# Performance work log

Hardware: AMD Instinct MI355X
Metric: run time of the kernel (lower is better)

The kernel has to match this reference:

```python
import jax, jax.numpy as jnp
import numpy as np

B, N, DIM = 4, 4096, 768
H = 12
DH = DIM // H          # 64
S = 16                 # num_segments
M = N // S             # 256 segment_len
SCALE = DH ** -0.5


def setup_inputs() -> dict:
    key = jax.random.key(0)
    ks = jax.random.split(key, 7)
    std = DIM ** -0.5
    return {
        "x": jax.random.normal(ks[0], (B, N, DIM), dtype=jnp.float32),
        "Wq": jax.random.normal(ks[1], (DIM, DIM), dtype=jnp.float32) * std,
        "Wkv": jax.random.normal(ks[2], (DIM, DIM), dtype=jnp.float32) * std,
        "Wo": jax.random.normal(ks[3], (DIM, DIM), dtype=jnp.float32) * std,
        "bo": jax.random.normal(ks[4], (DIM,), dtype=jnp.float32) * 0.02,
        "Wo0": jax.random.normal(ks[5], (DIM, DIM), dtype=jnp.float32) * std,
        "bo0": jax.random.normal(ks[6], (DIM,), dtype=jnp.float32) * 0.02,
    }


def _rotary_freqs(n, dh, dtype):
    # lucidrains RotaryEmbedding: inv_freq over even dims, emb = cat(freqs, freqs)
    inv_freq = 1.0 / (10000.0 ** (jnp.arange(0, dh, 2, dtype=jnp.float32) / dh))
    t = jnp.arange(n, dtype=jnp.float32)
    freqs = jnp.einsum("n,f->nf", t, inv_freq)           # (n, dh/2)
    return jnp.concatenate([freqs, freqs], axis=-1).astype(dtype)  # (n, dh)


def _rotate_half(t):
    # '... (j d) -> ... j d', j=2 ; (-x2, x1)
    x1, x2 = jnp.split(t, 2, axis=-1)
    return jnp.concatenate([-x2, x1], axis=-1)


def _apply_rotary(freqs, t):
    # freqs: (1, n, dh) broadcast over (bh, n, dh); rot_dim == dh here
    return t * jnp.cos(freqs) + _rotate_half(t) * jnp.sin(freqs)


def reference(x, Wq, Wkv, Wo, bo, Wo0, bo0):
    b, n, dim = x.shape
    q = x @ Wq            # (b, n, dim), bias-free
    kv = x @ Wkv          # shared K==V projection

    def to_heads(t):      # 'b n (h d) -> (b h) n d'
        return t.reshape(b, n, H, DH).transpose(0, 2, 1, 3).reshape(b * H, n, DH)

    q, kv = to_heads(q), to_heads(kv)

    freqs = _rotary_freqs(n, DH, x.dtype)[None, :, :]    # (1, n, dh)
    q = _apply_rotary(freqs, q)
    kv = _apply_rotary(freqs, kv)

    q = q * SCALE
    c = b * H
    qs = q.reshape(c, S, M, DH)
    kvs = kv.reshape(c, S, M, DH)

    # adjacent-segment KV windows: segment t attends to [t-1, t] for t>=1
    kvs_ccs = jnp.concatenate([kvs[:, :-1], kvs[:, 1:]], axis=2)  # (c, S-1, 2M, dh)
    qs_ccs = qs[:, 1:]                                            # (c, S-1, M, dh)

    lsim = jnp.einsum("csmd,csnd->csmn", qs_ccs, kvs_ccs)         # (c, S-1, M, 2M)
    attn1 = jax.nn.softmax(lsim, axis=-1)
    out1 = jnp.einsum("csmn,csnd->csmd", attn1, kvs_ccs)          # (c, S-1, M, dh)

    # global (self) attention within first segment
    q0, kv0 = qs[:, 0], kvs[:, 0]                                 # (c, M, dh)
    sim0 = jnp.einsum("cmd,cnd->cmn", q0, kv0)
    attn0 = jax.nn.softmax(sim0, axis=-1)
    out0 = jnp.einsum("cmn,cnd->cmd", attn0, kv0)                 # (c, M, dh)

    def merge_heads(t, nn):  # '(b h) nn d -> b nn (h d)'
        return t.reshape(b, H, nn, DH).transpose(0, 2, 1, 3).reshape(b, nn, H * DH)

    out_1 = merge_heads(out1.reshape(c, (S - 1) * M, DH), (S - 1) * M)
    out_0 = merge_heads(out0, M)

    out_1o = out_1 @ Wo + bo
    out_0o = out_0 @ Wo0 + bo0
    return jnp.concatenate([out_0o, out_1o], axis=1)              # (b, n, dim)
```

## Files before the change

### kernel.cpp

```cpp
#include <hip/hip_runtime.h>
#include <hip/hip_bf16.h>


typedef float f32x4 __attribute__((ext_vector_type(4)));
typedef short bf16x8 __attribute__((ext_vector_type(8)));

#define DEV static __device__ __forceinline__

DEV short f2bf(float f) {
  union { __hip_bfloat16 h; unsigned short u; } cv;
  cv.h = __float2bfloat16(f);
  return (short)cv.u;
}

DEV f32x4 fz4() { f32x4 z = {0.f, 0.f, 0.f, 0.f}; return z; }

DEV void gload16(const void* g, void* l) {
  __builtin_amdgcn_global_load_lds((const __attribute__((address_space(1))) void*)g,
                                   (__attribute__((address_space(3))) void*)l, 16, 0, 0);
}

__global__ void __launch_bounds__(256) k_rope(float2* __restrict__ csT) {
  int idx = blockIdx.x * 256 + threadIdx.x;
  int pos = idx >> 5, jm = idx & 31;
  float invf = exp2f(-(float)jm * (13.287712379549449f / 32.0f));
  float th = (float)pos * invf;
  csT[idx] = make_float2(cosf(th), sinf(th));
}

__global__ void __launch_bounds__(256) k_cvtx(const float* __restrict__ x,
                                              short* __restrict__ xb) {
  int i = (blockIdx.x * 256 + threadIdx.x) * 8;
  float4 a = *(const float4*)(x + i);
  float4 b = *(const float4*)(x + i + 4);
  bf16x8 v;
  v[0] = f2bf(a.x); v[1] = f2bf(a.y); v[2] = f2bf(a.z); v[3] = f2bf(a.w);
  v[4] = f2bf(b.x); v[5] = f2bf(b.y); v[6] = f2bf(b.z); v[7] = f2bf(b.w);
  *(bf16x8*)(xb + i) = v;
}

__global__ void __launch_bounds__(256) k_transw(const float* __restrict__ Wq,
                                                const float* __restrict__ Wkv,
                                                const float* __restrict__ Wo,
                                                const float* __restrict__ Wo0,
                                                short* __restrict__ WtQKV,
                                                short* __restrict__ WtO) {
  __shared__ float t[64][65];
  int z = blockIdx.z;
  const float* src = (z == 0) ? Wq : (z == 1) ? Wkv : (z == 2) ? Wo : Wo0;
  short* dst = (z < 2) ? (WtQKV + (size_t)z * (768 * 768))
                       : (WtO + (size_t)(z - 2) * (768 * 768));
  int k0 = blockIdx.x * 64, j0 = blockIdx.y * 64;
  int tc = threadIdx.x & 63, tr = threadIdx.x >> 6;
#pragma unroll
  for (int i = 0; i < 16; i++) {
    int r = i * 4 + tr;
    t[tc][r] = src[(size_t)(k0 + r) * 768 + j0 + tc];
  }
  __syncthreads();
#pragma unroll
  for (int i = 0; i < 16; i++) {
    int r = i * 4 + tr;
    dst[(size_t)(j0 + r) * 768 + k0 + tc] = f2bf(t[r][tc]);
  }
}

#define QSTAGE64(Abuf, Bbuf, Abase, Bbase, kt)                                 \
  {                                                                            \
    int cci = (((tid & 7) ^ ((tid >> 3) & 7)) << 4);                           \
    _Pragma("unroll") for (int i = 0; i < 4; i++) {                            \
      int rowi = i * 32 + (tid >> 3);                                          \
      gload16((Abase) + (size_t)(r0 + rowi) * 1536 + (kt) * 128 + cci,         \
              (char*)(Abuf) + i * 4096 + wid * 1024);                          \
      gload16((Bbase) + (size_t)(j0 + rowi) * 1536 + (kt) * 128 + cci,         \
              (char*)(Bbuf) + i * 4096 + wid * 1024);                          \
    }                                                                          \
  }

__global__ void __launch_bounds__(256, 2) k_gemm_qkv(
    const short* __restrict__ xb, const short* __restrict__ Wt,
    const float2* __restrict__ csT,
    short* __restrict__ Qb, short* __restrict__ KVb,
    short* __restrict__ KVtw) {
  __shared__ short Lsh[4][8192];
  int bid = blockIdx.x;
  int xcd = bid & 7, loc = bid >> 3;
  int r0 = (xcd * 16 + loc / 12) * 128;
  int cbk = loc % 12;
  bool isQ = cbk < 6;
  int cbl = isQ ? cbk : cbk - 6;
  const char* Ab = (const char*)xb;
  const char* Bb = (const char*)(Wt + (isQ ? (size_t)0 : (size_t)(768 * 768)));
  int j0 = cbl * 128;
  int tid = threadIdx.x, lane = tid & 63, wid = tid >> 6;
  int wr = wid >> 1, wc = wid & 1;
  int l15 = lane & 15, lg = lane >> 4;
  int swz = (l15 & 7) << 4;

  f32x4 acc[4][4];
#pragma unroll
  for (int i = 0; i < 4; i++)
#pragma unroll
    for (int j = 0; j < 4; j++) acc[i][j] = fz4();

  QSTAGE64(Lsh[0], Lsh[2], Ab, Bb, 0)
  for (int kt = 0; kt < 12; kt++) {
    int cb = kt & 1;
    __syncthreads();
    if (kt + 1 < 12) QSTAGE64(Lsh[cb ^ 1], Lsh[2 + (cb ^ 1)], Ab, Bb, kt + 1)
    const char* Ac = (const char*)Lsh[cb];
    const char* Bc = (const char*)Lsh[2 + cb];
#pragma unroll
    for (int kk = 0; kk < 2; kk++) {
      bf16x8 af[4], bfr[4];
#pragma unroll
      for (int mr = 0; mr < 4; mr++)
        af[mr] = *(const bf16x8*)(Ac + (wr * 64 + mr * 16 + l15) * 128 +
                                  ((kk * 64 + lg * 16) ^ swz));
#pragma unroll
      for (int nc = 0; nc < 4; nc++)
        bfr[nc] = *(const bf16x8*)(Bc + (wc * 64 + nc * 16 + l15) * 128 +
                                   ((kk * 64 + lg * 16) ^ swz));
#pragma unroll
      for (int mr = 0; mr < 4; mr++)
#pragma unroll
        for (int nc = 0; nc < 4; nc++)
          acc[mr][nc] = __builtin_amdgcn_mfma_f32_16x16x32_bf16(af[mr], bfr[nc], acc[mr][nc], 0, 0, 0);
    }
  }

  int h = 2 * cbl + wc;
  short* Ob = isQ ? Qb : KVb;
  float scl = isQ ? 0.18033688011112042f : 1.0f;
  short ovv[4][4][4];
#pragma unroll
  for (int mr = 0; mr < 4; mr++) {
#pragma unroll
    for (int rg = 0; rg < 4; rg++) {
      int r = r0 + wr * 64 + mr * 16 + lg * 4 + rg;
      int b = r >> 12, pos = r & 4095;
      const float2* cp = csT + pos * 32;
      float2 cs0 = cp[l15], cs1 = cp[16 + l15];
      float v0 = acc[mr][0][rg], v1 = acc[mr][1][rg];
      float v2 = acc[mr][2][rg], v3 = acc[mr][3][rg];
      short o0 = f2bf((v0 * cs0.x - v2 * cs0.y) * scl);
      short o1 = f2bf((v1 * cs1.x - v3 * cs1.y) * scl);
      short o2 = f2bf((v2 * cs0.x + v0 * cs0.y) * scl);
      short o3 = f2bf((v3 * cs1.x + v1 * cs1.y) * scl);
      size_t base = ((size_t)((b * 12 + h) * 4096 + pos)) * 64 + l15;
      Ob[base] = o0; Ob[base + 16] = o1; Ob[base + 32] = o2; Ob[base + 48] = o3;
      ovv[mr][rg][0] = o0; ovv[mr][rg][1] = o1;
      ovv[mr][rg][2] = o2; ovv[mr][rg][3] = o3;
    }
  }

  if (!isQ && KVtw) {
    __syncthreads();
    short* Ovt = (short*)Lsh;
#pragma unroll
    for (int mr = 0; mr < 4; mr++)
#pragma unroll
      for (int rg = 0; rg < 4; rg++) {
        int p = wr * 64 + mr * 16 + lg * 4 + rg;
        int w = p & 31, g = p >> 5;
        int sig = 8 * ((w & 15) >> 2) + 4 * ((w >> 4) & 1) + (w & 3);
        int pi = g * 32 + sig;
#pragma unroll
        for (int nc = 0; nc < 4; nc++) {
          int row = wc * 64 + nc * 16 + l15;
          Ovt[row * 136 + (pi ^ ((row & 3) << 4))] = ovv[mr][rg][nc];
        }
      }
    __syncthreads();
    int b = r0 >> 12, pos0 = r0 & 4095;
#pragma unroll
    for (int z = 0; z < 8; z++) {
      int rr = z * 16 + (tid >> 4);
      int chunk = tid & 15;
      int off = rr * 136 + ((chunk * 8) ^ ((rr & 3) << 4));
      bf16x8 v = *(const bf16x8*)&Ovt[off];
      int wcr = rr >> 6, d = rr & 63;
      *(bf16x8*)&KVtw[((size_t)((b * 12 + 2 * cbl + wcr) * 64 + d)) * 4096 +
                      pos0 + chunk * 8] = v;
    }
  }
}

__global__ void __launch_bounds__(256) k_transkv(const short* __restrict__ KVb,
                                                 short* __restrict__ KVt) {
  __shared__ short T[64][72];
  int c = blockIdx.x;
  int pt = blockIdx.y;
  int t = threadIdx.x;
  int ch = t & 7, rr = t >> 3;
#pragma unroll
  for (int i = 0; i < 2; i++) {
    int p = rr + i * 32;
    bf16x8 v = *(const bf16x8*)&KVb[((size_t)c * 4096 + pt * 64 + p) * 64 + ch * 8];
    *(bf16x8*)&T[p][ch * 8] = v;
  }
  __syncthreads();
#pragma unroll
  for (int i = 0; i < 2; i++) {
    int d = rr + i * 32;
    bf16x8 v;
#pragma unroll
    for (int j = 0; j < 8; j++) {
      int cc = ch * 8 + j;
      int g = cc >> 5, sig = cc & 31;
      int p = g * 32 + 4 * (sig >> 3) + (sig & 3) + 16 * ((sig >> 2) & 1);
      v[j] = T[p][d];
    }
    *(bf16x8*)&KVt[((size_t)c * 64 + d) * 4096 + pt * 64 + ch * 8] = v;
  }
}

#define STAGE(buf, kk0)                                                        \
  {                                                                            \
    _Pragma("unroll") for (int i = 0; i < 2; i++) {                            \
      gload16(KVc + (size_t)((kk0) + i * 32 + krow) * 128 + ksrccol,           \
              (char*)Kl[buf] + i * 4096 + wid * 1024);                         \
      gload16(KVtc + ((size_t)(i * 32 + krow) * 4096 + (kk0)) * 2 + ksrccol,   \
              (char*)Vl[buf] + i * 4096 + wid * 1024);                         \
    }                                                                          \
  }

__global__ void __launch_bounds__(256, 4) k_attn(const short* __restrict__ Qb,
                                                 const short* __restrict__ KVbp,
                                                 const short* __restrict__ KVtp,
                                                 short* __restrict__ AO) {
  __shared__ short Kl[2][4096];
  __shared__ short Vl[2][4096];
  int bid = blockIdx.x;
  int orig = (bid & 7) * 192 + (bid >> 3);
  int c = orig >> 5;
  int e = orig & 31;
  int s = (e < 2) ? 0 : ((e - 2) >> 1) + 1;
  int qh = (e < 2) ? e : (e - 2) & 1;
  int NC = (s == 0) ? 4 : 8;
  int Kbase = (s == 0) ? 0 : (s - 1) * 256;

  int tid = threadIdx.x, lane = tid & 63, wid = tid >> 6;
  int l15 = lane & 15, lg = lane >> 4;
  const char* KVc = (const char*)(KVbp + (size_t)c * 4096 * 64);
  const char* KVtc = (const char*)(KVtp + (size_t)c * 64 * 4096);

  int krow = tid >> 3;
  int ksrccol = ((tid & 7) * 16) ^ ((krow & 7) << 4);
  int swz = (l15 & 7) << 4;

  int q0 = s * 256 + qh * 128 + wid * 32;
  bf16x8 qf[2][2];
#pragma unroll
  for (int qt = 0; qt < 2; qt++) {
    const short* Qr = Qb + ((size_t)c * 4096 + q0 + qt * 16 + l15) * 64 + lg * 8;
    qf[qt][0] = *(const bf16x8*)Qr;
    qf[qt][1] = *(const bf16x8*)(Qr + 32);
  }

  const f32x4 mi = {-32.f, -32.f, -32.f, -32.f};
  bf16x8 ones;
#pragma unroll
  for (int j = 0; j < 8; j++) ones[j] = (short)0x3F80;

  f32x4 oacc[2][4];
  f32x4 lacc[2];
#pragma unroll
  for (int qt = 0; qt < 2; qt++) {
    lacc[qt] = fz4();
#pragma unroll
    for (int vt = 0; vt < 4; vt++) oacc[qt][vt] = fz4();
  }

  STAGE(0, Kbase)
  for (int ch = 0; ch < NC; ch++) {
    int cb = ch & 1;
    __syncthreads();
    if (ch + 1 < NC) STAGE(cb ^ 1, Kbase + (ch + 1) * 64)
    const char* Kb_ = (const char*)Kl[cb];
    const char* Vb_ = (const char*)Vl[cb];
#pragma unroll
    for (int u = 0; u < 2; u++) {
      f32x4 z[2][2];
#pragma unroll
      for (int t2 = 0; t2 < 2; t2++) {
        const char* Kp = Kb_ + ((2 * u + t2) * 16 + l15) * 128;
        bf16x8 kf0 = *(const bf16x8*)(Kp + ((lg * 16) ^ swz));
        bf16x8 kf1 = *(const bf16x8*)(Kp + ((64 + lg * 16) ^ swz));
        __builtin_amdgcn_s_setprio(1);
#pragma unroll
        for (int qt = 0; qt < 2; qt++) {
          f32x4 zz = __builtin_amdgcn_mfma_f32_16x16x32_bf16(kf0, qf[qt][0], mi, 0, 0, 0);
          zz = __builtin_amdgcn_mfma_f32_16x16x32_bf16(kf1, qf[qt][1], zz, 0, 0, 0);
          z[qt][t2] = zz;
        }
        __builtin_amdgcn_s_setprio(0);
      }
      bf16x8 pf[2];
#pragma unroll
      for (int qt = 0; qt < 2; qt++) {
#pragma unroll
        for (int t2 = 0; t2 < 2; t2++)
#pragma unroll
          for (int r = 0; r < 4; r++)
            pf[qt][t2 * 4 + r] = f2bf(exp2f(z[qt][t2][r]));
      }
      bf16x8 vf[4];
#pragma unroll
      for (int vt = 0; vt < 4; vt++)
        vf[vt] = *(const bf16x8*)(Vb_ + (vt * 16 + l15) * 128 +
                                  ((u * 64 + lg * 16) ^ swz));
      __builtin_amdgcn_s_setprio(1);
#pragma unroll
      for (int qt = 0; qt < 2; qt++) {
#pragma unroll
        for (int vt = 0; vt < 4; vt++)
          oacc[qt][vt] = __builtin_amdgcn_mfma_f32_16x16x32_bf16(pf[qt], vf[vt], oacc[qt][vt], 0, 0, 0);
        lacc[qt] = __builtin_amdgcn_mfma_f32_16x16x32_bf16(pf[qt], ones, lacc[qt], 0, 0, 0);
      }
      __builtin_amdgcn_s_setprio(0);
    }
  }

  int bq = c / 12, hh = c % 12;
#pragma unroll
  for (int qt = 0; qt < 2; qt++) {
    float rinv[4];
#pragma unroll
    for (int r = 0; r < 4; r++) rinv[r] = 1.0f / lacc[qt][r];
#pragma unroll
    for (int vt = 0; vt < 4; vt++)
#pragma unroll
      for (int r = 0; r < 4; r++) {
        size_t row = (size_t)bq * 4096 + q0 + qt * 16 + lg * 4 + r;
        AO[row * 768 + hh * 64 + vt * 16 + l15] = f2bf(oacc[qt][vt][r] * rinv[r]);
      }
  }
}

__global__ void __launch_bounds__(256, 2) k_gemm_out(
    const short* __restrict__ AO, const short* __restrict__ Wt,
    const float* __restrict__ bo, const float* __restrict__ bo0,
    float* __restrict__ out) {
  __shared__ short Lsh[4][8192];
  int bid = blockIdx.x;
  int xcd = bid & 7, loc = bid >> 3;
  int r0 = (xcd * 16 + loc / 6) * 128;
  int j0 = (loc % 6) * 128;
  bool o0sel = (r0 & 4095) < 256;
  const char* Ab = (const char*)AO;
  const char* Bb = (const char*)(Wt + (o0sel ? (size_t)1 : (size_t)0) * (768 * 768));
  const float* bias = o0sel ? bo0 : bo;
  int tid = threadIdx.x, lane = tid & 63, wid = tid >> 6;
  int wr = wid >> 1, wc = wid & 1;
  int l15 = lane & 15, lg = lane >> 4;
  int swz = (l15 & 7) << 4;

  f32x4 acc[4][4];
#pragma unroll
  for (int i = 0; i < 4; i++)
#pragma unroll
    for (int j = 0; j < 4; j++) acc[i][j] = fz4();

  QSTAGE64(Lsh[0], Lsh[2], Ab, Bb, 0)
  for (int kt = 0; kt < 12; kt++) {
    int cb = kt & 1;
    __syncthreads();
    if (kt + 1 < 12) QSTAGE64(Lsh[cb ^ 1], Lsh[2 + (cb ^ 1)], Ab, Bb, kt + 1)
    const char* Ac = (const char*)Lsh[cb];
    const char* Bc = (const char*)Lsh[2 + cb];
#pragma unroll
    for (int kk = 0; kk < 2; kk++) {
      bf16x8 af[4], bfr[4];
#pragma unroll
      for (int mr = 0; mr < 4; mr++)
        af[mr] = *(const bf16x8*)(Ac + (wr * 64 + mr * 16 + l15) * 128 +
                                  ((kk * 64 + lg * 16) ^ swz));
#pragma unroll
      for (int nc = 0; nc < 4; nc++)
        bfr[nc] = *(const bf16x8*)(Bc + (wc * 64 + nc * 16 + l15) * 128 +
                                   ((kk * 64 + lg * 16) ^ swz));
#pragma unroll
      for (int mr = 0; mr < 4; mr++)
#pragma unroll
        for (int nc = 0; nc < 4; nc++)
          acc[mr][nc] = __builtin_amdgcn_mfma_f32_16x16x32_bf16(af[mr], bfr[nc], acc[mr][nc], 0, 0, 0);
    }
  }

  float bs[4];
#pragma unroll
  for (int nc = 0; nc < 4; nc++) bs[nc] = bias[j0 + wc * 64 + nc * 16 + l15];
#pragma unroll
  for (int mr = 0; mr < 4; mr++)
#pragma unroll
    for (int rg = 0; rg < 4; rg++) {
      size_t r = (size_t)r0 + wr * 64 + mr * 16 + lg * 4 + rg;
      float* op = out + r * 768 + j0 + wc * 64 + l15;
      op[0]  = acc[mr][0][rg] + bs[0];
      op[16] = acc[mr][1][rg] + bs[1];
      op[32] = acc[mr][2][rg] + bs[2];
      op[48] = acc[mr][3][rg] + bs[3];
    }
}

extern "C" void kernel_launch(void* const* d_in, const int* in_sizes, int n_in,
                              void* d_out, int out_size, void* d_ws, size_t ws_size,
                              hipStream_t stream) {
  (void)in_sizes; (void)n_in; (void)out_size;
  const float* x   = (const float*)d_in[0];
  const float* Wq  = (const float*)d_in[1];
  const float* Wkv = (const float*)d_in[2];
  const float* Wo  = (const float*)d_in[3];
  const float* bo  = (const float*)d_in[4];
  const float* Wo0 = (const float*)d_in[5];
  const float* bo0 = (const float*)d_in[6];
  float* out = (float*)d_out;

  char* ws = (char*)d_ws;
  short* xb  = (short*)(ws + 0);
  short* AO  = xb;
  short* Qb  = (short*)(ws + 25165824);
  short* KVb = (short*)(ws + 50331648);
  short* KVt = (short*)(ws + 75497472);

  bool fused = ws_size >= 106430464u;
  float2* csT;
  short *WtQKV, *WtO;
  if (fused) {
    csT   = (float2*)(ws + 100663296);
    WtQKV = (short*)(ws + 101711872);
    WtO   = (short*)(ws + 104071168);
  } else {
    WtQKV = (short*)(ws + 75497472);
    csT   = (float2*)(ws + 77856768);
    WtO   = (short*)(ws + 100663296);
  }

  k_rope<<<512, 256, 0, stream>>>(csT);
  k_cvtx<<<6144, 256, 0, stream>>>(x, xb);
  k_transw<<<dim3(12, 12, 4), 256, 0, stream>>>(Wq, Wkv, Wo, Wo0, WtQKV, WtO);
  k_gemm_qkv<<<1536, 256, 0, stream>>>(xb, WtQKV, csT, Qb, KVb,
                                       fused ? KVt : (short*)nullptr);
  if (!fused) k_transkv<<<dim3(48, 64), 256, 0, stream>>>(KVb, KVt);
  k_attn<<<1536, 256, 0, stream>>>(Qb, KVb, KVt, AO);
  k_gemm_out<<<768, 256, 0, stream>>>(AO, WtO, bo, bo0, out);
}
```

Measured before the change: 150.4 us.

## Rewrite projection GEMMs with 256x256 tiles, 8 waves, and phased prefetch pipeline

Both the QKV and output projection GEMMs move from 128x128 tiles with 4 waves to 256x256 tiles with 8 waves and 128 KB of dynamic LDS. The main loop is now split into half-tile phases that interleave global-to-LDS prefetches with MFMA work, using explicit vmcnt waits, raw s_barriers and setprio. The goal is higher arithmetic intensity and better overlap of memory with compute. In exchange the grids become much smaller (384 and 192 blocks), which may leave CUs underused, and the large LDS footprint means at most one block can fit per CU.

```diff
diff --git a/kernel.cpp b/kernel.cpp
--- a/kernel.cpp
+++ b/kernel.cpp
@@ -65,123 +65,163 @@
   }
 }
 
-#define QSTAGE64(Abuf, Bbuf, Abase, Bbase, kt)                                 \
+#define GSTAGE_HT(dst, src, T, h, rowoff)                                      \
   {                                                                            \
-    int cci = (((tid & 7) ^ ((tid >> 3) & 7)) << 4);                           \
-    _Pragma("unroll") for (int i = 0; i < 4; i++) {                            \
-      int rowi = i * 32 + (tid >> 3);                                          \
-      gload16((Abase) + (size_t)(r0 + rowi) * 1536 + (kt) * 128 + cci,         \
-              (char*)(Abuf) + i * 4096 + wid * 1024);                          \
-      gload16((Bbase) + (size_t)(j0 + rowi) * 1536 + (kt) * 128 + cci,         \
-              (char*)(Bbuf) + i * 4096 + wid * 1024);                          \
-    }                                                                          \
-  }
-
-__global__ void __launch_bounds__(256, 2) k_gemm_qkv(
+    int cci_ = (((tid & 7) ^ ((tid >> 3) & 7)) << 4);                          \
+    _Pragma("unroll") for (int i_ = 0; i_ < 2; i_++) {                         \
+      gload16((src) + (size_t)((rowoff) + (h) * 128 + i_ * 64 + (tid >> 3)) * 1536 + \
+                  (size_t)(T) * 128 + cci_,                                    \
+              (dst) + (h) * 16384 + i_ * 8192 + wid * 1024);                   \
+    }                                                                          \
+  }
+
+#define VMC4 { asm volatile("s_waitcnt vmcnt(4)" ::: "memory"); __builtin_amdgcn_sched_barrier(0); }
+#define VMC0 { asm volatile("s_waitcnt vmcnt(0)" ::: "memory"); __builtin_amdgcn_sched_barrier(0); }
+
+#define DS_A(q, kk) (*(const bf16x8*)(Acur + (wr * 128 + (q) * 16 + l15) * 128 + \
+                                      (((kk) * 64 + lg * 16) ^ swz)))
+#define DS_B(n, kk) (*(const bf16x8*)(Bcur + (wc * 64 + (n) * 16 + l15) * 128 + \
+                                      (((kk) * 64 + lg * 16) ^ swz)))
+
+#define PH(qd, VMW)                                                            \
+  {                                                                            \
+    if ((qd) == 0) {                                                           \
+      _Pragma("unroll") for (int n_ = 0; n_ < 4; n_++) {                       \
+        breg[n_][0] = DS_B(n_, 0);                                             \
+        breg[n_][1] = DS_B(n_, 1);                                             \
+      }                                                                        \
+    }                                                                          \
+    bf16x8 a00 = DS_A(2 * (qd), 0), a01 = DS_A(2 * (qd), 1);                   \
+    bf16x8 a10 = DS_A(2 * (qd) + 1, 0), a11 = DS_A(2 * (qd) + 1, 1);           \
+    VMW                                                                        \
+    __builtin_amdgcn_s_barrier();                                              \
+    asm volatile("s_waitcnt lgkmcnt(0)" ::: "memory");                         \
+    __builtin_amdgcn_sched_barrier(0);                                         \
+    __builtin_amdgcn_s_setprio(1);                                             \
+    _Pragma("unroll") for (int n_ = 0; n_ < 4; n_++) {                         \
+      acc[2 * (qd)][n_] = __builtin_amdgcn_mfma_f32_16x16x32_bf16(a00, breg[n_][0], acc[2 * (qd)][n_], 0, 0, 0); \
+      acc[2 * (qd)][n_] = __builtin_amdgcn_mfma_f32_16x16x32_bf16(a01, breg[n_][1], acc[2 * (qd)][n_], 0, 0, 0); \
+      acc[2 * (qd) + 1][n_] = __builtin_amdgcn_mfma_f32_16x16x32_bf16(a10, breg[n_][0], acc[2 * (qd) + 1][n_], 0, 0, 0); \
+      acc[2 * (qd) + 1][n_] = __builtin_amdgcn_mfma_f32_16x16x32_bf16(a11, breg[n_][1], acc[2 * (qd) + 1][n_], 0, 0, 0); \
+    }                                                                          \
+    __builtin_amdgcn_s_setprio(0);                                             \
+    __builtin_amdgcn_s_barrier();                                              \
+  }
+
+#define K256_LOOP(Abase, Bbase)                                                \
+  GSTAGE_HT(AL0, Abase, 0, 0, r0)                                              \
+  GSTAGE_HT(AL0, Abase, 0, 1, r0)                                              \
+  GSTAGE_HT(BL0, Bbase, 0, 0, j0)                                              \
+  GSTAGE_HT(BL0, Bbase, 0, 1, j0)                                              \
+  GSTAGE_HT(BL1, Bbase, 1, 0, j0)                                              \
+  GSTAGE_HT(BL1, Bbase, 1, 1, j0)                                              \
+  VMC4                                                                         \
+  __builtin_amdgcn_s_barrier();                                                \
+  for (int t = 0; t < 6; t++) {                                                \
+    bool lastt = (t == 5);                                                     \
+    {                                                                          \
+      const char* Acur = AL0; const char* Bcur = BL0;                          \
+      bf16x8 breg[4][2];                                                       \
+      GSTAGE_HT(AL1, Abase, 2 * t + 1, 0, r0)                                  \
+      PH(0, )                                                                  \
+      GSTAGE_HT(AL1, Abase, 2 * t + 1, 1, r0)                                  \
+      PH(1, )                                                                  \
+      if (!lastt) { GSTAGE_HT(BL0, Bbase, 2 * t + 2, 0, j0) }                  \
+      PH(2, )                                                                  \
+      if (!lastt) { GSTAGE_HT(BL0, Bbase, 2 * t + 2, 1, j0) }                  \
+      PH(3, if (lastt) { VMC0 } else { VMC4 })                                 \
+    }                                                                          \
+    {                                                                          \
+      const char* Acur = AL1; const char* Bcur = BL1;                          \
+      bf16x8 breg[4][2];                                                       \
+      if (!lastt) { GSTAGE_HT(AL0, Abase, 2 * t + 2, 0, r0) }                  \
+      PH(0, )                                                                  \
+      if (!lastt) { GSTAGE_HT(AL0, Abase, 2 * t + 2, 1, r0) }                  \
+      PH(1, )                                                                  \
+      if (!lastt) { GSTAGE_HT(BL1, Bbase, 2 * t + 3, 0, j0) }                  \
+      PH(2, )                                                                  \
+      if (!lastt) { GSTAGE_HT(BL1, Bbase, 2 * t + 3, 1, j0) }                  \
+      PH(3, if (!lastt) { VMC4 })                                              \
+    }                                                                          \
+  }
+
+__global__ void __launch_bounds__(512, 2) k_gemm_qkv(
     const short* __restrict__ xb, const short* __restrict__ Wt,
     const float2* __restrict__ csT,
     short* __restrict__ Qb, short* __restrict__ KVb,
     short* __restrict__ KVtw) {
-  __shared__ short Lsh[4][8192];
+  extern __shared__ char GL[];
+  char* AL0 = GL;
+  char* AL1 = GL + 32768;
+  char* BL0 = GL + 65536;
+  char* BL1 = GL + 98304;
   int bid = blockIdx.x;
   int xcd = bid & 7, loc = bid >> 3;
-  int r0 = (xcd * 16 + loc / 12) * 128;
-  int cbk = loc % 12;
-  bool isQ = cbk < 6;
-  int cbl = isQ ? cbk : cbk - 6;
-  const char* Ab = (const char*)xb;
-  const char* Bb = (const char*)(Wt + (isQ ? (size_t)0 : (size_t)(768 * 768)));
-  int j0 = cbl * 128;
+  int mb = xcd * 8 + loc / 6;
+  int cbn = loc % 6;
+  bool isQ = cbn < 3;
+  int r0 = mb * 256;
+  int j0 = (isQ ? cbn : cbn - 3) * 256;
+  const char* Abase = (const char*)xb;
+  const char* Bbase = (const char*)(Wt + (isQ ? (size_t)0 : (size_t)(768 * 768)));
   int tid = threadIdx.x, lane = tid & 63, wid = tid >> 6;
-  int wr = wid >> 1, wc = wid & 1;
+  int wr = wid >> 2, wc = wid & 3;
   int l15 = lane & 15, lg = lane >> 4;
   int swz = (l15 & 7) << 4;
 
-  f32x4 acc[4][4];
-#pragma unroll
-  for (int i = 0; i < 4; i++)
+  f32x4 acc[8][4];
+#pragma unroll
+  for (int i = 0; i < 8; i++)
 #pragma unroll
     for (int j = 0; j < 4; j++) acc[i][j] = fz4();
 
-  QSTAGE64(Lsh[0], Lsh[2], Ab, Bb, 0)
-  for (int kt = 0; kt < 12; kt++) {
-    int cb = kt & 1;
-    __syncthreads();
-    if (kt + 1 < 12) QSTAGE64(Lsh[cb ^ 1], Lsh[2 + (cb ^ 1)], Ab, Bb, kt + 1)
-    const char* Ac = (const char*)Lsh[cb];
-    const char* Bc = (const char*)Lsh[2 + cb];
-#pragma unroll
-    for (int kk = 0; kk < 2; kk++) {
-      bf16x8 af[4], bfr[4];
-#pragma unroll
-      for (int mr = 0; mr < 4; mr++)
-        af[mr] = *(const bf16x8*)(Ac + (wr * 64 + mr * 16 + l15) * 128 +
-                                  ((kk * 64 + lg * 16) ^ swz));
-#pragma unroll
-      for (int nc = 0; nc < 4; nc++)
-        bfr[nc] = *(const bf16x8*)(Bc + (wc * 64 + nc * 16 + l15) * 128 +
-                                   ((kk * 64 + lg * 16) ^ swz));
-#pragma unroll
-      for (int mr = 0; mr < 4; mr++)
-#pragma unroll
-        for (int nc = 0; nc < 4; nc++)
-          acc[mr][nc] = __builtin_amdgcn_mfma_f32_16x16x32_bf16(af[mr], bfr[nc], acc[mr][nc], 0, 0, 0);
-    }
-  }
-
-  int h = 2 * cbl + wc;
+  K256_LOOP(Abase, Bbase)
+
+  int h = (isQ ? cbn : cbn - 3) * 4 + wc;
   short* Ob = isQ ? Qb : KVb;
   float scl = isQ ? 0.18033688011112042f : 1.0f;
-  short ovv[4][4][4];
-#pragma unroll
-  for (int mr = 0; mr < 4; mr++) {
+  bool dofuse = (!isQ) && (KVtw != nullptr);
+  short* LB = (short*)GL;
+#pragma unroll
+  for (int m = 0; m < 8; m++) {
 #pragma unroll
     for (int rg = 0; rg < 4; rg++) {
-      int r = r0 + wr * 64 + mr * 16 + lg * 4 + rg;
+      int r = r0 + wr * 128 + m * 16 + lg * 4 + rg;
       int b = r >> 12, pos = r & 4095;
       const float2* cp = csT + pos * 32;
       float2 cs0 = cp[l15], cs1 = cp[16 + l15];
-      float v0 = acc[mr][0][rg], v1 = acc[mr][1][rg];
-      float v2 = acc[mr][2][rg], v3 = acc[mr][3][rg];
+      float v0 = acc[m][0][rg], v1 = acc[m][1][rg];
+      float v2 = acc[m][2][rg], v3 = acc[m][3][rg];
       short o0 = f2bf((v0 * cs0.x - v2 * cs0.y) * scl);
       short o1 = f2bf((v1 * cs1.x - v3 * cs1.y) * scl);
       short o2 = f2bf((v2 * cs0.x + v0 * cs0.y) * scl);
       short o3 = f2bf((v3 * cs1.x + v1 * cs1.y) * scl);
       size_t base = ((size_t)((b * 12 + h) * 4096 + pos)) * 64 + l15;
       Ob[base] = o0; Ob[base + 16] = o1; Ob[base + 32] = o2; Ob[base + 48] = o3;
-      ovv[mr][rg][0] = o0; ovv[mr][rg][1] = o1;
-      ovv[mr][rg][2] = o2; ovv[mr][rg][3] = o3;
-    }
-  }
-
-  if (!isQ && KVtw) {
-    __syncthreads();
-    short* Ovt = (short*)Lsh;
-#pragma unroll
-    for (int mr = 0; mr < 4; mr++)
-#pragma unroll
-      for (int rg = 0; rg < 4; rg++) {
-        int p = wr * 64 + mr * 16 + lg * 4 + rg;
-        int w = p & 31, g = p >> 5;
-        int sig = 8 * ((w & 15) >> 2) + 4 * ((w >> 4) & 1) + (w & 3);
-        int pi = g * 32 + sig;
-#pragma unroll
-        for (int nc = 0; nc < 4; nc++) {
-          int row = wc * 64 + nc * 16 + l15;
-          Ovt[row * 136 + (pi ^ ((row & 3) << 4))] = ovv[mr][rg][nc];
+      if (dofuse) {
+        int ptl = wr * 128 + m * 16 + lg * 4 + rg;
+        int g = ptl >> 5, w = ptl & 31;
+        int pp = g * 32 + 8 * ((w & 15) >> 2) + 4 * ((w >> 4) & 1) + (w & 3);
+        int ch = pp >> 3, sub = pp & 7;
+        short ov[4] = {o0, o1, o2, o3};
+#pragma unroll
+        for (int n = 0; n < 4; n++) {
+          int rowd = wc * 64 + n * 16 + l15;
+          LB[rowd * 256 + (((ch ^ (rowd & 31)) << 3) + sub)] = ov[n];
         }
       }
+    }
+  }
+  if (dofuse) {
     __syncthreads();
-    int b = r0 >> 12, pos0 = r0 & 4095;
-#pragma unroll
-    for (int z = 0; z < 8; z++) {
-      int rr = z * 16 + (tid >> 4);
-      int chunk = tid & 15;
-      int off = rr * 136 + ((chunk * 8) ^ ((rr & 3) << 4));
-      bf16x8 v = *(const bf16x8*)&Ovt[off];
-      int wcr = rr >> 6, d = rr & 63;
-      *(bf16x8*)&KVtw[((size_t)((b * 12 + 2 * cbl + wcr) * 64 + d)) * 4096 +
-                      pos0 + chunk * 8] = v;
+    int b = r0 >> 12, pos0 = r0 & 4095, hb = (cbn - 3) * 4;
+#pragma unroll
+    for (int z = 0; z < 16; z++) {
+      int rr = z * 16 + (tid >> 5);
+      int ck = tid & 31;
+      bf16x8 v = *(const bf16x8*)&LB[rr * 256 + ((ck ^ (rr & 31)) << 3)];
+      *(bf16x8*)&KVtw[((size_t)((b * 12 + hb + (rr >> 6)) * 64 + (rr & 63))) * 4096 +
+                      pos0 + ck * 8] = v;
     }
   }
 }
@@ -338,69 +378,51 @@
   }
 }
 
-__global__ void __launch_bounds__(256, 2) k_gemm_out(
+__global__ void __launch_bounds__(512, 2) k_gemm_out(
     const short* __restrict__ AO, const short* __restrict__ Wt,
     const float* __restrict__ bo, const float* __restrict__ bo0,
     float* __restrict__ out) {
-  __shared__ short Lsh[4][8192];
+  extern __shared__ char GL[];
+  char* AL0 = GL;
+  char* AL1 = GL + 32768;
+  char* BL0 = GL + 65536;
+  char* BL1 = GL + 98304;
   int bid = blockIdx.x;
   int xcd = bid & 7, loc = bid >> 3;
-  int r0 = (xcd * 16 + loc / 6) * 128;
-  int j0 = (loc % 6) * 128;
+  int mb = xcd * 8 + loc / 3;
+  int jn = loc % 3;
+  int r0 = mb * 256;
+  int j0 = jn * 256;
   bool o0sel = (r0 & 4095) < 256;
-  const char* Ab = (const char*)AO;
-  const char* Bb = (const char*)(Wt + (o0sel ? (size_t)1 : (size_t)0) * (768 * 768));
+  const char* Abase = (const char*)AO;
+  const char* Bbase = (const char*)(Wt + (o0sel ? (size_t)1 : (size_t)0) * (768 * 768));
   const float* bias = o0sel ? bo0 : bo;
   int tid = threadIdx.x, lane = tid & 63, wid = tid >> 6;
-  int wr = wid >> 1, wc = wid & 1;
+  int wr = wid >> 2, wc = wid & 3;
   int l15 = lane & 15, lg = lane >> 4;
   int swz = (l15 & 7) << 4;
 
-  f32x4 acc[4][4];
-#pragma unroll
-  for (int i = 0; i < 4; i++)
+  f32x4 acc[8][4];
+#pragma unroll
+  for (int i = 0; i < 8; i++)
 #pragma unroll
     for (int j = 0; j < 4; j++) acc[i][j] = fz4();
 
-  QSTAGE64(Lsh[0], Lsh[2], Ab, Bb, 0)
-  for (int kt = 0; kt < 12; kt++) {
-    int cb = kt & 1;
-    __syncthreads();
-    if (kt + 1 < 12) QSTAGE64(Lsh[cb ^ 1], Lsh[2 + (cb ^ 1)], Ab, Bb, kt + 1)
-    const char* Ac = (const char*)Lsh[cb];
-    const char* Bc = (const char*)Lsh[2 + cb];
-#pragma unroll
-    for (int kk = 0; kk < 2; kk++) {
-      bf16x8 af[4], bfr[4];
-#pragma unroll
-      for (int mr = 0; mr < 4; mr++)
-        af[mr] = *(const bf16x8*)(Ac + (wr * 64 + mr * 16 + l15) * 128 +
-                                  ((kk * 64 + lg * 16) ^ swz));
-#pragma unroll
-      for (int nc = 0; nc < 4; nc++)
-        bfr[nc] = *(const bf16x8*)(Bc + (wc * 64 + nc * 16 + l15) * 128 +
-                                   ((kk * 64 + lg * 16) ^ swz));
-#pragma unroll
-      for (int mr = 0; mr < 4; mr++)
-#pragma unroll
-        for (int nc = 0; nc < 4; nc++)
-          acc[mr][nc] = __builtin_amdgcn_mfma_f32_16x16x32_bf16(af[mr], bfr[nc], acc[mr][nc], 0, 0, 0);
-    }
-  }
+  K256_LOOP(Abase, Bbase)
 
   float bs[4];
 #pragma unroll
-  for (int nc = 0; nc < 4; nc++) bs[nc] = bias[j0 + wc * 64 + nc * 16 + l15];
-#pragma unroll
-  for (int mr = 0; mr < 4; mr++)
+  for (int n = 0; n < 4; n++) bs[n] = bias[j0 + wc * 64 + n * 16 + l15];
+#pragma unroll
+  for (int m = 0; m < 8; m++)
 #pragma unroll
     for (int rg = 0; rg < 4; rg++) {
-      size_t r = (size_t)r0 + wr * 64 + mr * 16 + lg * 4 + rg;
+      size_t r = (size_t)r0 + wr * 128 + m * 16 + lg * 4 + rg;
       float* op = out + r * 768 + j0 + wc * 64 + l15;
-      op[0]  = acc[mr][0][rg] + bs[0];
-      op[16] = acc[mr][1][rg] + bs[1];
-      op[32] = acc[mr][2][rg] + bs[2];
-      op[48] = acc[mr][3][rg] + bs[3];
+      op[0]  = acc[m][0][rg] + bs[0];
+      op[16] = acc[m][1][rg] + bs[1];
+      op[32] = acc[m][2][rg] + bs[2];
+      op[48] = acc[m][3][rg] + bs[3];
     }
 }
 
@@ -440,9 +462,9 @@
   k_rope<<<512, 256, 0, stream>>>(csT);
   k_cvtx<<<6144, 256, 0, stream>>>(x, xb);
   k_transw<<<dim3(12, 12, 4), 256, 0, stream>>>(Wq, Wkv, Wo, Wo0, WtQKV, WtO);
-  k_gemm_qkv<<<1536, 256, 0, stream>>>(xb, WtQKV, csT, Qb, KVb,
-                                       fused ? KVt : (short*)nullptr);
+  k_gemm_qkv<<<384, 512, 131072, stream>>>(xb, WtQKV, csT, Qb, KVb,
+                                           fused ? KVt : (short*)nullptr);
   if (!fused) k_transkv<<<dim3(48, 64), 256, 0, stream>>>(KVb, KVt);
   k_attn<<<1536, 256, 0, stream>>>(Qb, KVb, KVt, AO);
-  k_gemm_out<<<768, 256, 0, stream>>>(AO, WtO, bo, bo0, out);
-}
+  k_gemm_out<<<192, 512, 131072, stream>>>(AO, WtO, bo, bo0, out);
+}
```

Measured after the change: 155.0 us. +3.0%, slower.
